# Optimization experiments

Measured on AMD Instinct MI355X. Metric: run time of the kernel, lower is better.

## Reference

```python
import jax, jax.numpy as jnp
import numpy as np

NUM_HEADS = 16

def setup_inputs() -> dict:
    key = jax.random.key(0)
    ks = jax.random.split(key, 9)
    B, S, H = 2, 2048, 1024
    sc = 0.02
    return {
        "x":  jax.random.normal(ks[0], (B, S, H), jnp.float32),
        "Wq": jax.random.normal(ks[1], (H, H), jnp.float32) * sc,
        "bq": jnp.zeros((H,), jnp.float32),
        "Wk": jax.random.normal(ks[2], (H, H), jnp.float32) * sc,
        "bk": jnp.zeros((H,), jnp.float32),
        "Wv": jax.random.normal(ks[3], (H, H), jnp.float32) * sc,
        "bv": jnp.zeros((H,), jnp.float32),
        "Wo": jax.random.normal(ks[4], (H, H), jnp.float32) * sc,
        "bo": jnp.zeros((H,), jnp.float32),
    }

def _split_heads(t, nh):
    B, S, H = t.shape
    return t.reshape(B, S, nh, H // nh).transpose(0, 2, 1, 3)  # [B, nh, S, hd]

def reference(x, Wq, bq, Wk, bk, Wv, bv, Wo, bo):
    # mask_type == 'gaussian', dropout = 0 (eval), return_weights = False
    B, S, H = x.shape
    nh = NUM_HEADS
    q = _split_heads(x @ Wq + bq, nh)  # [B, nh, S, hd]
    k = _split_heads(x @ Wk + bk, nh)
    v = _split_heads(x @ Wv + bv, nh)
    dif = q - k  # elementwise, as in the original
    # exp(-dif @ dif^T / 2)
    score = jnp.exp(-0.5 * jnp.einsum('bhqd,bhkd->bhqk', dif, dif))
    # gaussian mask: 1 strictly above the diagonal, 0 on/below (faithful to source)
    mask = jnp.triu(jnp.ones((S, S), x.dtype), k=1)
    prob = score * mask  # [B, nh, S, S]
    ctx = jnp.einsum('bhqk,bhkd->bhqd', prob, v)  # [B, nh, S, hd]
    ctx = ctx.transpose(0, 2, 1, 3).reshape(B, S, H)
    return ctx @ Wo + bo
```

## Files before the change

### kernel.cpp

```cpp
#include <hip/hip_runtime.h>
#include <math.h>

constexpr int SEQ  = 2048;
constexpr int HID  = 1024;
constexpr int MTOT = 4096;
constexpr int BH   = 32;

typedef _Float16 f16;
typedef _Float16 f16x8 __attribute__((ext_vector_type(8)));
typedef float    f32x4 __attribute__((ext_vector_type(4)));

__global__ __launch_bounds__(256) void cvt_x(const float* __restrict__ in,
                                             f16* __restrict__ out) {
    const int i = (blockIdx.x * 256 + threadIdx.x) * 4;
    float4 v = *(const float4*)(in + i);
    f16 o[4] = {(f16)v.x, (f16)v.y, (f16)v.z, (f16)v.w};
    *(ushort4*)(out + i) = *(ushort4*)o;
}

template<int SUB>
__global__ __launch_bounds__(256) void cvt_wT(const float* __restrict__ W,
                                              const float* __restrict__ W2,
                                              f16* __restrict__ WT) {
    __shared__ f16 T[64][72];
    const int k0 = blockIdx.x * 64, n0 = blockIdx.y * 64;
    const int t = threadIdx.x;
    const int r  = t >> 4;
    const int c4 = (t & 15) * 4;
#pragma unroll
    for (int rr = 0; rr < 64; rr += 16) {
        float4 w = *(const float4*)(W + (size_t)(k0 + rr + r) * HID + n0 + c4);
        if (SUB) {
            float4 w2 = *(const float4*)(W2 + (size_t)(k0 + rr + r) * HID + n0 + c4);
            w.x -= w2.x; w.y -= w2.y; w.z -= w2.z; w.w -= w2.w;
        }
        T[c4 + 0][rr + r] = (f16)w.x;
        T[c4 + 1][rr + r] = (f16)w.y;
        T[c4 + 2][rr + r] = (f16)w.z;
        T[c4 + 3][rr + r] = (f16)w.w;
    }
    __syncthreads();
#pragma unroll
    for (int pp = 0; pp < 2; pp++) {
        const int nr = pp * 32 + (t >> 3);
        const int kc = (t & 7) * 8;
        *(uint4*)(WT + (size_t)(n0 + nr) * HID + k0 + kc) = *(uint4*)(&T[nr][kc]);
    }
}

__global__ __launch_bounds__(256) void proj_gemm(const f16* __restrict__ A,
                                                 const f16* __restrict__ WqkT,
                                                 const f16* __restrict__ WvT,
                                                 const float* __restrict__ bq,
                                                 const float* __restrict__ bk,
                                                 const float* __restrict__ bv,
                                                 f16* __restrict__ dif,
                                                 f16* __restrict__ vT) {
    __shared__ f16 As[128 * 72];
    __shared__ f16 Bs[128 * 72];
    const int t = threadIdx.x;
    const int m0  = blockIdx.x * 128;
    const int n0g = blockIdx.y * 128;
    const bool isv = (n0g >= HID);
    const f16* BT = isv ? WvT : WqkT;
    const int n0 = n0g & (HID - 1);
    const int w = t >> 6, l = t & 63, quad = l >> 4, ln = l & 15;
    const int wm = (w >> 1) * 64, wn = (w & 1) * 64;
    const int srow = t >> 1, shalf = (t & 1) * 32;

    const f16* pa = A  + (size_t)(m0 + srow) * HID + shalf;
    const f16* pb = BT + (size_t)(n0 + srow) * HID + shalf;

    uint4 ar0 = *(const uint4*)(pa),      ar1 = *(const uint4*)(pa + 8);
    uint4 ar2 = *(const uint4*)(pa + 16), ar3 = *(const uint4*)(pa + 24);
    uint4 br0 = *(const uint4*)(pb),      br1 = *(const uint4*)(pb + 8);
    uint4 br2 = *(const uint4*)(pb + 16), br3 = *(const uint4*)(pb + 24);

    f32x4 acc[4][4] = {};

    for (int k0 = 0; k0 < HID; k0 += 64) {
        __syncthreads();
        f16* da = As + srow * 72 + shalf;
        f16* db = Bs + srow * 72 + shalf;
        *(uint4*)(da)      = ar0; *(uint4*)(da + 8)  = ar1;
        *(uint4*)(da + 16) = ar2; *(uint4*)(da + 24) = ar3;
        *(uint4*)(db)      = br0; *(uint4*)(db + 8)  = br1;
        *(uint4*)(db + 16) = br2; *(uint4*)(db + 24) = br3;
        __syncthreads();
        if (k0 + 64 < HID) {
            const f16* qa = pa + k0 + 64;
            const f16* qb = pb + k0 + 64;
            ar0 = *(const uint4*)(qa);      ar1 = *(const uint4*)(qa + 8);
            ar2 = *(const uint4*)(qa + 16); ar3 = *(const uint4*)(qa + 24);
            br0 = *(const uint4*)(qb);      br1 = *(const uint4*)(qb + 8);
            br2 = *(const uint4*)(qb + 16); br3 = *(const uint4*)(qb + 24);
        }
#pragma unroll
        for (int kh = 0; kh < 2; kh++) {
            f16x8 af[4], bf[4];
#pragma unroll
            for (int mt = 0; mt < 4; mt++)
                af[mt] = *(const f16x8*)(As + (wm + mt * 16 + ln) * 72 + kh * 32 + quad * 8);
#pragma unroll
            for (int nt = 0; nt < 4; nt++)
                bf[nt] = *(const f16x8*)(Bs + (wn + nt * 16 + ln) * 72 + kh * 32 + quad * 8);
#pragma unroll
            for (int mt = 0; mt < 4; mt++)
#pragma unroll
                for (int nt = 0; nt < 4; nt++)
                    acc[mt][nt] = __builtin_amdgcn_mfma_f32_16x16x32_f16(
                        af[mt], bf[nt], acc[mt][nt], 0, 0, 0);
        }
    }

#pragma unroll
    for (int mt = 0; mt < 4; mt++) {
#pragma unroll
        for (int nt = 0; nt < 4; nt++) {
            const int nl = n0 + wn + nt * 16 + ln;
            const int m_base = m0 + wm + mt * 16 + quad * 4;
            const int h = nl >> 6, e = nl & 63;
            if (!isv) {
                const float bb = bq[nl] - bk[nl];
#pragma unroll
                for (int r = 0; r < 4; r++) {
                    const int m = m_base + r;
                    const int b = m >> 11, s = m & 2047;
                    dif[((size_t)(b * 16 + h) * SEQ + s) * 64 + e] =
                        (f16)(acc[mt][nt][r] + bb);
                }
            } else {
                const float bb = bv[nl];
                const int b = m_base >> 11, s0 = m_base & 2047;
                f16 o[4];
#pragma unroll
                for (int r = 0; r < 4; r++) o[r] = (f16)(acc[mt][nt][r] + bb);
                *(ushort4*)(&vT[((size_t)(b * 16 + h) * 64 + e) * SEQ + s0]) =
                    *(ushort4*)o;
            }
        }
    }
}

__global__ __launch_bounds__(256) void out_gemm(const f16* __restrict__ C0,
                                                const f16* __restrict__ C1,
                                                const f16* __restrict__ WoT,
                                                const float* __restrict__ bo,
                                                float* __restrict__ out) {
    __shared__ f16 As[128 * 72];
    __shared__ f16 Bs[64 * 72];
    const int t = threadIdx.x;
    const int m0 = blockIdx.x * 128, n0 = blockIdx.y * 64;
    const int w = t >> 6, l = t & 63, quad = l >> 4, ln = l & 15;
    const int wm = (w >> 1) * 64, wn = (w & 1) * 32;
    const int arow = t >> 1, ahalf = (t & 1) * 32;
    const int brow = t >> 2, boff = (t & 3) * 16;

    const f16* pa0 = C0  + (size_t)(m0 + arow) * HID + ahalf;
    const f16* pa1 = C1  + (size_t)(m0 + arow) * HID + ahalf;
    const f16* pb  = WoT + (size_t)(n0 + brow) * HID + boff;

    f16x8 a0 = *(const f16x8*)(pa0)      + *(const f16x8*)(pa1);
    f16x8 a1 = *(const f16x8*)(pa0 + 8)  + *(const f16x8*)(pa1 + 8);
    f16x8 a2 = *(const f16x8*)(pa0 + 16) + *(const f16x8*)(pa1 + 16);
    f16x8 a3 = *(const f16x8*)(pa0 + 24) + *(const f16x8*)(pa1 + 24);
    uint4 b0 = *(const uint4*)(pb), b1 = *(const uint4*)(pb + 8);

    f32x4 acc[4][2] = {};

    for (int k0 = 0; k0 < HID; k0 += 64) {
        __syncthreads();
        f16* da = As + arow * 72 + ahalf;
        *(f16x8*)(da)      = a0; *(f16x8*)(da + 8)  = a1;
        *(f16x8*)(da + 16) = a2; *(f16x8*)(da + 24) = a3;
        f16* db = Bs + brow * 72 + boff;
        *(uint4*)(db) = b0; *(uint4*)(db + 8) = b1;
        __syncthreads();
        if (k0 + 64 < HID) {
            const int kn = k0 + 64;
            a0 = *(const f16x8*)(pa0 + kn)      + *(const f16x8*)(pa1 + kn);
            a1 = *(const f16x8*)(pa0 + kn + 8)  + *(const f16x8*)(pa1 + kn + 8);
            a2 = *(const f16x8*)(pa0 + kn + 16) + *(const f16x8*)(pa1 + kn + 16);
            a3 = *(const f16x8*)(pa0 + kn + 24) + *(const f16x8*)(pa1 + kn + 24);
            b0 = *(const uint4*)(pb + kn); b1 = *(const uint4*)(pb + kn + 8);
        }
#pragma unroll
        for (int kh = 0; kh < 2; kh++) {
            f16x8 af[4], bf[2];
#pragma unroll
            for (int mt = 0; mt < 4; mt++)
                af[mt] = *(const f16x8*)(As + (wm + mt * 16 + ln) * 72 + kh * 32 + quad * 8);
#pragma unroll
            for (int nt = 0; nt < 2; nt++)
                bf[nt] = *(const f16x8*)(Bs + (wn + nt * 16 + ln) * 72 + kh * 32 + quad * 8);
#pragma unroll
            for (int mt = 0; mt < 4; mt++)
#pragma unroll
                for (int nt = 0; nt < 2; nt++)
                    acc[mt][nt] = __builtin_amdgcn_mfma_f32_16x16x32_f16(
                        af[mt], bf[nt], acc[mt][nt], 0, 0, 0);
        }
    }

#pragma unroll
    for (int mt = 0; mt < 4; mt++)
#pragma unroll
        for (int nt = 0; nt < 2; nt++) {
            const int n = n0 + wn + nt * 16 + ln;
            const float bb = bo[n];
            const int m_base = m0 + wm + mt * 16 + quad * 4;
#pragma unroll
            for (int r = 0; r < 4; r++)
                out[(size_t)(m_base + r) * HID + n] =
                    acc[mt][nt][r] * 65536.0f + bb;
        }
}

__global__ __launch_bounds__(256) void attn_f16(const f16* __restrict__ dif,
                                                const f16* __restrict__ vT,
                                                f16* __restrict__ ctx0,
                                                f16* __restrict__ ctx1) {
    __shared__ f16 Qs[64 * 72];
    __shared__ f16 Ks[64 * 72];
    __shared__ f16 Vs[64 * 72];
    __shared__ f16 Ps[64 * 72];

    const int pq = blockIdx.x, bh = blockIdx.y, ks = blockIdx.z;
    f16* Cout = ks ? ctx1 : ctx0;
    const f16* D  = dif + (size_t)bh * SEQ * 64;
    const f16* VT = vT  + (size_t)bh * 64 * SEQ;
    const int b = bh >> 4, h = bh & 15;
    const int t = threadIdx.x, w = t >> 6, l = t & 63, quad = l >> 4, ln = l & 15;
    const int ve = t >> 2, vc = (t & 3) * 16;

    for (int half = 0; half < 2; half++) {
        const int qt = half ? (31 - pq) : pq;
        const int i0 = qt * 64;
        __syncthreads();

#pragma unroll
        for (int rr = 0; rr < 2; rr++) {
            const int o = rr * 2048 + t * 8;
            uint4 v = *(const uint4*)(D + i0 * 64 + o);
            *(uint4*)(Qs + (o >> 6) * 72 + (o & 63)) = v;
        }

        f32x4 acc[4] = {};
        const int kt0 = qt + ks;

        uint4 kr0, kr1, vr0, vr1;
        if (kt0 < 32) {
            const int j0 = kt0 * 64;
            kr0 = *(const uint4*)(D + j0 * 64 + t * 8);
            kr1 = *(const uint4*)(D + j0 * 64 + 2048 + t * 8);
            vr0 = *(const uint4*)(VT + (size_t)ve * SEQ + j0 + vc);
            vr1 = *(const uint4*)(VT + (size_t)ve * SEQ + j0 + vc + 8);
        }

        for (int kt = kt0; kt < 32; kt += 2) {
            __syncthreads();

            {
                const int o0 = t * 8, o1 = 2048 + t * 8;
                *(uint4*)(Ks + (o0 >> 6) * 72 + (o0 & 63)) = kr0;
                *(uint4*)(Ks + (o1 >> 6) * 72 + (o1 & 63)) = kr1;
                *(uint4*)(Vs + ve * 72 + vc)     = vr0;
                *(uint4*)(Vs + ve * 72 + vc + 8) = vr1;
            }
            __syncthreads();

            if (kt + 2 < 32) {
                const int j2 = (kt + 2) * 64;
                kr0 = *(const uint4*)(D + j2 * 64 + t * 8);
                kr1 = *(const uint4*)(D + j2 * 64 + 2048 + t * 8);
                vr0 = *(const uint4*)(VT + (size_t)ve * SEQ + j2 + vc);
                vr1 = *(const uint4*)(VT + (size_t)ve * SEQ + j2 + vc + 8);
            }

            f32x4 s[4] = {};
#pragma unroll
            for (int kh = 0; kh < 2; kh++) {
                f16x8 a = *(const f16x8*)(Qs + (w * 16 + ln) * 72 + kh * 32 + quad * 8);
#pragma unroll
                for (int nt = 0; nt < 4; nt++) {
                    f16x8 bfr = *(const f16x8*)(Ks + (nt * 16 + ln) * 72 + kh * 32 + quad * 8);
                    s[nt] = __builtin_amdgcn_mfma_f32_16x16x32_f16(a, bfr, s[nt], 0, 0, 0);
                }
            }

            const bool full = (kt > qt);
#pragma unroll
            for (int nt = 0; nt < 4; nt++)
#pragma unroll
                for (int r = 0; r < 4; r++) {
                    const int iloc = w * 16 + quad * 4 + r;
                    const int jloc = nt * 16 + ln;
                    float p = (full || (jloc > iloc))
                                  ? fminf(__expf(-0.5f * s[nt][r]) * 0x1p-16f, 60000.0f)
                                  : 0.0f;
                    Ps[iloc * 72 + jloc] = (f16)p;
                }

#pragma unroll
            for (int kh = 0; kh < 2; kh++) {
                f16x8 a = *(const f16x8*)(Ps + (w * 16 + ln) * 72 + kh * 32 + quad * 8);
#pragma unroll
                for (int nt = 0; nt < 4; nt++) {
                    f16x8 bfr = *(const f16x8*)(Vs + (nt * 16 + ln) * 72 + kh * 32 + quad * 8);
                    acc[nt] = __builtin_amdgcn_mfma_f32_16x16x32_f16(a, bfr, acc[nt], 0, 0, 0);
                }
            }
        }

#pragma unroll
        for (int nt = 0; nt < 4; nt++)
#pragma unroll
            for (int r = 0; r < 4; r++) {
                const int iloc = w * 16 + quad * 4 + r;
                Cout[(size_t)(b * SEQ + i0 + iloc) * HID + h * 64 + nt * 16 + ln] =
                    (f16)acc[nt][r];
            }
    }
}

extern "C" void kernel_launch(void* const* d_in, const int* in_sizes, int n_in,
                              void* d_out, int out_size, void* d_ws, size_t ws_size,
                              hipStream_t stream) {
    const float* x  = (const float*)d_in[0];
    const float* Wq = (const float*)d_in[1];
    const float* bq = (const float*)d_in[2];
    const float* Wk = (const float*)d_in[3];
    const float* bk = (const float*)d_in[4];
    const float* Wv = (const float*)d_in[5];
    const float* bv = (const float*)d_in[6];
    const float* Wo = (const float*)d_in[7];
    const float* bo = (const float*)d_in[8];
    float* out = (float*)d_out;

    char* ws = (char*)d_ws;
    f16* xh   = (f16*)(ws);
    f16* WqkT = (f16*)(ws + (8 << 20));
    f16* WvT  = (f16*)(ws + (10 << 20));
    f16* WoT  = (f16*)(ws + (12 << 20));
    f16* dif  = (f16*)(ws + (14 << 20));
    f16* vT   = (f16*)(ws + (22 << 20));
    f16* ctx0 = (f16*)(ws + (30 << 20));
    f16* ctx1 = (f16*)(ws + (38 << 20));

    cvt_x<<<MTOT * HID / 1024, 256, 0, stream>>>(x, xh);
    dim3 wtg(16, 16);
    cvt_wT<1><<<wtg, 256, 0, stream>>>(Wq, Wk, WqkT);
    cvt_wT<0><<<wtg, 256, 0, stream>>>(Wv, nullptr, WvT);
    cvt_wT<0><<<wtg, 256, 0, stream>>>(Wo, nullptr, WoT);

    proj_gemm<<<dim3(MTOT / 128, 16), 256, 0, stream>>>(xh, WqkT, WvT,
                                                        bq, bk, bv, dif, vT);
    attn_f16<<<dim3(16, BH, 2), 256, 0, stream>>>(dif, vT, ctx0, ctx1);
    out_gemm<<<dim3(MTOT / 128, 16), 256, 0, stream>>>(ctx0, ctx1, WoT, bo, out);
}
```

Before: 191.4 us.

## Use 128-row query tiles with three-way key split in attention

```diff
diff --git a/kernel.cpp b/kernel.cpp
--- a/kernel.cpp
+++ b/kernel.cpp
@@ -18,11 +18,19 @@
     *(ushort4*)(out + i) = *(ushort4*)o;
 }
 
-template<int SUB>
-__global__ __launch_bounds__(256) void cvt_wT(const float* __restrict__ W,
-                                              const float* __restrict__ W2,
-                                              f16* __restrict__ WT) {
+__global__ __launch_bounds__(256) void cvt_w_all(const float* __restrict__ Wq,
+                                                 const float* __restrict__ Wk,
+                                                 const float* __restrict__ Wv,
+                                                 const float* __restrict__ Wo,
+                                                 f16* __restrict__ WqkT,
+                                                 f16* __restrict__ WvT,
+                                                 f16* __restrict__ WoT) {
     __shared__ f16 T[64][72];
+    const int z = blockIdx.z;
+    const float* W  = (z == 0) ? Wq : (z == 1) ? Wv : Wo;
+    const float* W2 = Wk;
+    f16* WT = (z == 0) ? WqkT : (z == 1) ? WvT : WoT;
+
     const int k0 = blockIdx.x * 64, n0 = blockIdx.y * 64;
     const int t = threadIdx.x;
     const int r  = t >> 4;
@@ -30,7 +38,7 @@
 #pragma unroll
     for (int rr = 0; rr < 64; rr += 16) {
         float4 w = *(const float4*)(W + (size_t)(k0 + rr + r) * HID + n0 + c4);
-        if (SUB) {
+        if (z == 0) {
             float4 w2 = *(const float4*)(W2 + (size_t)(k0 + rr + r) * HID + n0 + c4);
             w.x -= w2.x; w.y -= w2.y; w.z -= w2.z; w.w -= w2.w;
         }
@@ -144,6 +152,7 @@
 
 __global__ __launch_bounds__(256) void out_gemm(const f16* __restrict__ C0,
                                                 const f16* __restrict__ C1,
+                                                const f16* __restrict__ C2,
                                                 const f16* __restrict__ WoT,
                                                 const float* __restrict__ bo,
                                                 float* __restrict__ out) {
@@ -158,12 +167,13 @@
 
     const f16* pa0 = C0  + (size_t)(m0 + arow) * HID + ahalf;
     const f16* pa1 = C1  + (size_t)(m0 + arow) * HID + ahalf;
+    const f16* pa2 = C2  + (size_t)(m0 + arow) * HID + ahalf;
     const f16* pb  = WoT + (size_t)(n0 + brow) * HID + boff;
 
-    f16x8 a0 = *(const f16x8*)(pa0)      + *(const f16x8*)(pa1);
-    f16x8 a1 = *(const f16x8*)(pa0 + 8)  + *(const f16x8*)(pa1 + 8);
-    f16x8 a2 = *(const f16x8*)(pa0 + 16) + *(const f16x8*)(pa1 + 16);
-    f16x8 a3 = *(const f16x8*)(pa0 + 24) + *(const f16x8*)(pa1 + 24);
+    f16x8 a0 = *(const f16x8*)(pa0)      + *(const f16x8*)(pa1)      + *(const f16x8*)(pa2);
+    f16x8 a1 = *(const f16x8*)(pa0 + 8)  + *(const f16x8*)(pa1 + 8)  + *(const f16x8*)(pa2 + 8);
+    f16x8 a2 = *(const f16x8*)(pa0 + 16) + *(const f16x8*)(pa1 + 16) + *(const f16x8*)(pa2 + 16);
+    f16x8 a3 = *(const f16x8*)(pa0 + 24) + *(const f16x8*)(pa1 + 24) + *(const f16x8*)(pa2 + 24);
     uint4 b0 = *(const uint4*)(pb), b1 = *(const uint4*)(pb + 8);
 
     f32x4 acc[4][2] = {};
@@ -178,10 +188,10 @@
         __syncthreads();
         if (k0 + 64 < HID) {
             const int kn = k0 + 64;
-            a0 = *(const f16x8*)(pa0 + kn)      + *(const f16x8*)(pa1 + kn);
-            a1 = *(const f16x8*)(pa0 + kn + 8)  + *(const f16x8*)(pa1 + kn + 8);
-            a2 = *(const f16x8*)(pa0 + kn + 16) + *(const f16x8*)(pa1 + kn + 16);
-            a3 = *(const f16x8*)(pa0 + kn + 24) + *(const f16x8*)(pa1 + kn + 24);
+            a0 = *(const f16x8*)(pa0 + kn)      + *(const f16x8*)(pa1 + kn)      + *(const f16x8*)(pa2 + kn);
+            a1 = *(const f16x8*)(pa0 + kn + 8)  + *(const f16x8*)(pa1 + kn + 8)  + *(const f16x8*)(pa2 + kn + 8);
+            a2 = *(const f16x8*)(pa0 + kn + 16) + *(const f16x8*)(pa1 + kn + 16) + *(const f16x8*)(pa2 + kn + 16);
+            a3 = *(const f16x8*)(pa0 + kn + 24) + *(const f16x8*)(pa1 + kn + 24) + *(const f16x8*)(pa2 + kn + 24);
             b0 = *(const uint4*)(pb + kn); b1 = *(const uint4*)(pb + kn + 8);
         }
 #pragma unroll
@@ -219,14 +229,16 @@
 __global__ __launch_bounds__(256) void attn_f16(const f16* __restrict__ dif,
                                                 const f16* __restrict__ vT,
                                                 f16* __restrict__ ctx0,
-                                                f16* __restrict__ ctx1) {
-    __shared__ f16 Qs[64 * 72];
-    __shared__ f16 Ks[64 * 72];
-    __shared__ f16 Vs[64 * 72];
-    __shared__ f16 Ps[64 * 72];
+                                                f16* __restrict__ ctx1,
+                                                f16* __restrict__ ctx2) {
+    constexpr int LP = 72;
+    __shared__ f16 KV[2 * 64 * LP];
+    __shared__ f16 Ps[128 * LP];
+    f16* Ks = KV;
+    f16* Vs = KV + 64 * LP;
 
     const int pq = blockIdx.x, bh = blockIdx.y, ks = blockIdx.z;
-    f16* Cout = ks ? ctx1 : ctx0;
+    f16* Cout = (ks == 0) ? ctx0 : (ks == 1) ? ctx1 : ctx2;
     const f16* D  = dif + (size_t)bh * SEQ * 64;
     const f16* VT = vT  + (size_t)bh * 64 * SEQ;
     const int b = bh >> 4, h = bh & 15;
@@ -234,92 +246,121 @@
     const int ve = t >> 2, vc = (t & 3) * 16;
 
     for (int half = 0; half < 2; half++) {
-        const int qt = half ? (31 - pq) : pq;
-        const int i0 = qt * 64;
-        __syncthreads();
-
-#pragma unroll
-        for (int rr = 0; rr < 2; rr++) {
-            const int o = rr * 2048 + t * 8;
-            uint4 v = *(const uint4*)(D + i0 * 64 + o);
-            *(uint4*)(Qs + (o >> 6) * 72 + (o & 63)) = v;
-        }
-
-        f32x4 acc[4] = {};
-        const int kt0 = qt + ks;
+        const int qt = half ? (15 - pq) : pq;
+        const int i0 = qt * 128;
+        __syncthreads();
+
+#pragma unroll
+        for (int c = 0; c < 4; c++) {
+            const int o = c * 2048 + t * 8;
+            *(uint4*)(&KV[o]) = *(const uint4*)(D + (size_t)i0 * 64 + o);
+        }
+        __syncthreads();
+        f16x8 aq[2][2];
+#pragma unroll
+        for (int st = 0; st < 2; st++)
+#pragma unroll
+            for (int kh = 0; kh < 2; kh++)
+                aq[st][kh] = *(const f16x8*)(&KV[(w * 32 + st * 16 + ln) * 64
+                                                + kh * 32 + quad * 8]);
+        __syncthreads();
+
+        f32x4 acc[2][4] = {};
+        const int kt0 = qt * 2 + ks;
 
         uint4 kr0, kr1, vr0, vr1;
         if (kt0 < 32) {
             const int j0 = kt0 * 64;
-            kr0 = *(const uint4*)(D + j0 * 64 + t * 8);
-            kr1 = *(const uint4*)(D + j0 * 64 + 2048 + t * 8);
+            kr0 = *(const uint4*)(D + (size_t)j0 * 64 + t * 8);
+            kr1 = *(const uint4*)(D + (size_t)j0 * 64 + 2048 + t * 8);
             vr0 = *(const uint4*)(VT + (size_t)ve * SEQ + j0 + vc);
             vr1 = *(const uint4*)(VT + (size_t)ve * SEQ + j0 + vc + 8);
         }
 
-        for (int kt = kt0; kt < 32; kt += 2) {
+        for (int kt = kt0; kt < 32; kt += 3) {
+            const int j0 = kt * 64;
             __syncthreads();
 
             {
                 const int o0 = t * 8, o1 = 2048 + t * 8;
-                *(uint4*)(Ks + (o0 >> 6) * 72 + (o0 & 63)) = kr0;
-                *(uint4*)(Ks + (o1 >> 6) * 72 + (o1 & 63)) = kr1;
-                *(uint4*)(Vs + ve * 72 + vc)     = vr0;
-                *(uint4*)(Vs + ve * 72 + vc + 8) = vr1;
+                *(uint4*)(&Ks[(o0 >> 6) * LP + (o0 & 63)]) = kr0;
+                *(uint4*)(&Ks[(o1 >> 6) * LP + (o1 & 63)]) = kr1;
+                *(uint4*)(&Vs[ve * LP + vc])     = vr0;
+                *(uint4*)(&Vs[ve * LP + vc + 8]) = vr1;
             }
             __syncthreads();
 
-            if (kt + 2 < 32) {
-                const int j2 = (kt + 2) * 64;
-                kr0 = *(const uint4*)(D + j2 * 64 + t * 8);
-                kr1 = *(const uint4*)(D + j2 * 64 + 2048 + t * 8);
+            if (kt + 3 < 32) {
+                const int j2 = (kt + 3) * 64;
+                kr0 = *(const uint4*)(D + (size_t)j2 * 64 + t * 8);
+                kr1 = *(const uint4*)(D + (size_t)j2 * 64 + 2048 + t * 8);
                 vr0 = *(const uint4*)(VT + (size_t)ve * SEQ + j2 + vc);
                 vr1 = *(const uint4*)(VT + (size_t)ve * SEQ + j2 + vc + 8);
             }
 
-            f32x4 s[4] = {};
+            const int gi0 = i0 + w * 32;
+            const bool live0 = (j0 + 63) > gi0;
+            const bool live1 = (j0 + 63) > (gi0 + 16);
+
+            f32x4 s[2][4] = {};
+#pragma unroll
+            for (int kh = 0; kh < 2; kh++)
+#pragma unroll
+                for (int nt = 0; nt < 4; nt++) {
+                    f16x8 bk = *(const f16x8*)(&Ks[(nt * 16 + ln) * LP + kh * 32 + quad * 8]);
+                    if (live0) s[0][nt] = __builtin_amdgcn_mfma_f32_16x16x32_f16(
+                                              aq[0][kh], bk, s[0][nt], 0, 0, 0);
+                    if (live1) s[1][nt] = __builtin_amdgcn_mfma_f32_16x16x32_f16(
+                                              aq[1][kh], bk, s[1][nt], 0, 0, 0);
+                }
+
+#pragma unroll
+            for (int st = 0; st < 2; st++) {
+                const bool live = st ? live1 : live0;
+                if (!live) continue;
+                const int gs = gi0 + st * 16;
+                const bool nomask = j0 > gs + 15;
+#pragma unroll
+                for (int nt = 0; nt < 4; nt++)
+#pragma unroll
+                    for (int r = 0; r < 4; r++) {
+                        float p = __expf(fmaf(s[st][nt][r], -0.5f, -11.090354888959125f));
+                        p = fminf(p, 60000.0f);
+                        if (!nomask) {
+                            const int gi = gs + quad * 4 + r;
+                            const int gj = j0 + nt * 16 + ln;
+                            p = (gj > gi) ? p : 0.0f;
+                        }
+                        Ps[(w * 32 + st * 16 + quad * 4 + r) * LP + nt * 16 + ln] = (f16)p;
+                    }
+            }
+
 #pragma unroll
             for (int kh = 0; kh < 2; kh++) {
-                f16x8 a = *(const f16x8*)(Qs + (w * 16 + ln) * 72 + kh * 32 + quad * 8);
+                f16x8 ap0, ap1;
+                if (live0) ap0 = *(const f16x8*)(&Ps[(w * 32 + ln) * LP + kh * 32 + quad * 8]);
+                if (live1) ap1 = *(const f16x8*)(&Ps[(w * 32 + 16 + ln) * LP + kh * 32 + quad * 8]);
 #pragma unroll
                 for (int nt = 0; nt < 4; nt++) {
-                    f16x8 bfr = *(const f16x8*)(Ks + (nt * 16 + ln) * 72 + kh * 32 + quad * 8);
-                    s[nt] = __builtin_amdgcn_mfma_f32_16x16x32_f16(a, bfr, s[nt], 0, 0, 0);
+                    f16x8 bv = *(const f16x8*)(&Vs[(nt * 16 + ln) * LP + kh * 32 + quad * 8]);
+                    if (live0) acc[0][nt] = __builtin_amdgcn_mfma_f32_16x16x32_f16(
+                                                ap0, bv, acc[0][nt], 0, 0, 0);
+                    if (live1) acc[1][nt] = __builtin_amdgcn_mfma_f32_16x16x32_f16(
+                                                ap1, bv, acc[1][nt], 0, 0, 0);
                 }
             }
-
-            const bool full = (kt > qt);
+        }
+
+#pragma unroll
+        for (int st = 0; st < 2; st++)
 #pragma unroll
             for (int nt = 0; nt < 4; nt++)
 #pragma unroll
                 for (int r = 0; r < 4; r++) {
-                    const int iloc = w * 16 + quad * 4 + r;
-                    const int jloc = nt * 16 + ln;
-                    float p = (full || (jloc > iloc))
-                                  ? fminf(__expf(-0.5f * s[nt][r]) * 0x1p-16f, 60000.0f)
-                                  : 0.0f;
-                    Ps[iloc * 72 + jloc] = (f16)p;
+                    const int iloc = w * 32 + st * 16 + quad * 4 + r;
+                    Cout[(size_t)(b * SEQ + i0 + iloc) * HID + h * 64 + nt * 16 + ln] =
+                        (f16)acc[st][nt][r];
                 }
-
-#pragma unroll
-            for (int kh = 0; kh < 2; kh++) {
-                f16x8 a = *(const f16x8*)(Ps + (w * 16 + ln) * 72 + kh * 32 + quad * 8);
-#pragma unroll
-                for (int nt = 0; nt < 4; nt++) {
-                    f16x8 bfr = *(const f16x8*)(Vs + (nt * 16 + ln) * 72 + kh * 32 + quad * 8);
-                    acc[nt] = __builtin_amdgcn_mfma_f32_16x16x32_f16(a, bfr, acc[nt], 0, 0, 0);
-                }
-            }
-        }
-
-#pragma unroll
-        for (int nt = 0; nt < 4; nt++)
-#pragma unroll
-            for (int r = 0; r < 4; r++) {
-                const int iloc = w * 16 + quad * 4 + r;
-                Cout[(size_t)(b * SEQ + i0 + iloc) * HID + h * 64 + nt * 16 + ln] =
-                    (f16)acc[nt][r];
-            }
     }
 }
 
@@ -346,15 +387,13 @@
     f16* vT   = (f16*)(ws + (22 << 20));
     f16* ctx0 = (f16*)(ws + (30 << 20));
     f16* ctx1 = (f16*)(ws + (38 << 20));
+    f16* ctx2 = xh;
 
     cvt_x<<<MTOT * HID / 1024, 256, 0, stream>>>(x, xh);
-    dim3 wtg(16, 16);
-    cvt_wT<1><<<wtg, 256, 0, stream>>>(Wq, Wk, WqkT);
-    cvt_wT<0><<<wtg, 256, 0, stream>>>(Wv, nullptr, WvT);
-    cvt_wT<0><<<wtg, 256, 0, stream>>>(Wo, nullptr, WoT);
+    cvt_w_all<<<dim3(16, 16, 3), 256, 0, stream>>>(Wq, Wk, Wv, Wo, WqkT, WvT, WoT);
 
     proj_gemm<<<dim3(MTOT / 128, 16), 256, 0, stream>>>(xh, WqkT, WvT,
                                                         bq, bk, bv, dif, vT);
-    attn_f16<<<dim3(16, BH, 2), 256, 0, stream>>>(dif, vT, ctx0, ctx1);
-    out_gemm<<<dim3(MTOT / 128, 16), 256, 0, stream>>>(ctx0, ctx1, WoT, bo, out);
-}
+    attn_f16<<<dim3(8, BH, 3), 256, 0, stream>>>(dif, vT, ctx0, ctx1, ctx2);
+    out_gemm<<<dim3(MTOT / 128, 16), 256, 0, stream>>>(ctx0, ctx1, ctx2, WoT, bo, out);
+}
```

After: 205.5 us. +7.3%, slower.

## Merge conversion kernels into one launch and double-buffer LDS in GEMMs

Applied to the files above, without the earlier changes.

```diff
diff --git a/kernel.cpp b/kernel.cpp
--- a/kernel.cpp
+++ b/kernel.cpp
@@ -10,28 +10,43 @@
 typedef _Float16 f16x8 __attribute__((ext_vector_type(8)));
 typedef float    f32x4 __attribute__((ext_vector_type(4)));
 
-__global__ __launch_bounds__(256) void cvt_x(const float* __restrict__ in,
-                                             f16* __restrict__ out) {
-    const int i = (blockIdx.x * 256 + threadIdx.x) * 4;
-    float4 v = *(const float4*)(in + i);
-    f16 o[4] = {(f16)v.x, (f16)v.y, (f16)v.z, (f16)v.w};
-    *(ushort4*)(out + i) = *(ushort4*)o;
-}
-
-template<int SUB>
-__global__ __launch_bounds__(256) void cvt_wT(const float* __restrict__ W,
-                                              const float* __restrict__ W2,
-                                              f16* __restrict__ WT) {
+__global__ __launch_bounds__(256) void prep(const float* __restrict__ x,
+                                            const float* __restrict__ Wq,
+                                            const float* __restrict__ Wk,
+                                            const float* __restrict__ Wv,
+                                            const float* __restrict__ Wo,
+                                            f16* __restrict__ xh,
+                                            f16* __restrict__ WqkT,
+                                            f16* __restrict__ WvT,
+                                            f16* __restrict__ WoT) {
     __shared__ f16 T[64][72];
+    const int z = blockIdx.z;
+    const int t = threadIdx.x;
+
+    if (z == 3) {
+        const int chunk = blockIdx.y * 16 + blockIdx.x;
+        const float* src = x + (size_t)chunk * 16384;
+        f16* dst = xh + (size_t)chunk * 16384;
+#pragma unroll
+        for (int it = 0; it < 16; it++) {
+            const int i = it * 1024 + t * 4;
+            float4 v = *(const float4*)(src + i);
+            f16 o[4] = {(f16)v.x, (f16)v.y, (f16)v.z, (f16)v.w};
+            *(ushort4*)(dst + i) = *(ushort4*)o;
+        }
+        return;
+    }
+
+    const float* W  = (z == 0) ? Wq : (z == 1) ? Wv : Wo;
+    f16* WT = (z == 0) ? WqkT : (z == 1) ? WvT : WoT;
     const int k0 = blockIdx.x * 64, n0 = blockIdx.y * 64;
-    const int t = threadIdx.x;
     const int r  = t >> 4;
     const int c4 = (t & 15) * 4;
 #pragma unroll
     for (int rr = 0; rr < 64; rr += 16) {
         float4 w = *(const float4*)(W + (size_t)(k0 + rr + r) * HID + n0 + c4);
-        if (SUB) {
-            float4 w2 = *(const float4*)(W2 + (size_t)(k0 + rr + r) * HID + n0 + c4);
+        if (z == 0) {
+            float4 w2 = *(const float4*)(Wk + (size_t)(k0 + rr + r) * HID + n0 + c4);
             w.x -= w2.x; w.y -= w2.y; w.z -= w2.z; w.w -= w2.w;
         }
         T[c4 + 0][rr + r] = (f16)w.x;
@@ -56,8 +71,8 @@
                                                  const float* __restrict__ bv,
                                                  f16* __restrict__ dif,
                                                  f16* __restrict__ vT) {
-    __shared__ f16 As[128 * 72];
-    __shared__ f16 Bs[128 * 72];
+    __shared__ f16 As[2][128 * 72];
+    __shared__ f16 Bs[2][128 * 72];
     const int t = threadIdx.x;
     const int m0  = blockIdx.x * 128;
     const int n0g = blockIdx.y * 128;
@@ -77,11 +92,11 @@
     uint4 br2 = *(const uint4*)(pb + 16), br3 = *(const uint4*)(pb + 24);
 
     f32x4 acc[4][4] = {};
+    int buf = 0;
 
     for (int k0 = 0; k0 < HID; k0 += 64) {
-        __syncthreads();
-        f16* da = As + srow * 72 + shalf;
-        f16* db = Bs + srow * 72 + shalf;
+        f16* da = As[buf] + srow * 72 + shalf;
+        f16* db = Bs[buf] + srow * 72 + shalf;
         *(uint4*)(da)      = ar0; *(uint4*)(da + 8)  = ar1;
         *(uint4*)(da + 16) = ar2; *(uint4*)(da + 24) = ar3;
         *(uint4*)(db)      = br0; *(uint4*)(db + 8)  = br1;
@@ -100,10 +115,10 @@
             f16x8 af[4], bf[4];
 #pragma unroll
             for (int mt = 0; mt < 4; mt++)
-                af[mt] = *(const f16x8*)(As + (wm + mt * 16 + ln) * 72 + kh * 32 + quad * 8);
+                af[mt] = *(const f16x8*)(As[buf] + (wm + mt * 16 + ln) * 72 + kh * 32 + quad * 8);
 #pragma unroll
             for (int nt = 0; nt < 4; nt++)
-                bf[nt] = *(const f16x8*)(Bs + (wn + nt * 16 + ln) * 72 + kh * 32 + quad * 8);
+                bf[nt] = *(const f16x8*)(Bs[buf] + (wn + nt * 16 + ln) * 72 + kh * 32 + quad * 8);
 #pragma unroll
             for (int mt = 0; mt < 4; mt++)
 #pragma unroll
@@ -111,6 +126,7 @@
                     acc[mt][nt] = __builtin_amdgcn_mfma_f32_16x16x32_f16(
                         af[mt], bf[nt], acc[mt][nt], 0, 0, 0);
         }
+        buf ^= 1;
     }
 
 #pragma unroll
@@ -147,8 +163,8 @@
                                                 const f16* __restrict__ WoT,
                                                 const float* __restrict__ bo,
                                                 float* __restrict__ out) {
-    __shared__ f16 As[128 * 72];
-    __shared__ f16 Bs[64 * 72];
+    __shared__ f16 As[2][128 * 72];
+    __shared__ f16 Bs[2][64 * 72];
     const int t = threadIdx.x;
     const int m0 = blockIdx.x * 128, n0 = blockIdx.y * 64;
     const int w = t >> 6, l = t & 63, quad = l >> 4, ln = l & 15;
@@ -167,13 +183,13 @@
     uint4 b0 = *(const uint4*)(pb), b1 = *(const uint4*)(pb + 8);
 
     f32x4 acc[4][2] = {};
+    int buf = 0;
 
     for (int k0 = 0; k0 < HID; k0 += 64) {
-        __syncthreads();
-        f16* da = As + arow * 72 + ahalf;
+        f16* da = As[buf] + arow * 72 + ahalf;
         *(f16x8*)(da)      = a0; *(f16x8*)(da + 8)  = a1;
         *(f16x8*)(da + 16) = a2; *(f16x8*)(da + 24) = a3;
-        f16* db = Bs + brow * 72 + boff;
+        f16* db = Bs[buf] + brow * 72 + boff;
         *(uint4*)(db) = b0; *(uint4*)(db + 8) = b1;
         __syncthreads();
         if (k0 + 64 < HID) {
@@ -189,10 +205,10 @@
             f16x8 af[4], bf[2];
 #pragma unroll
             for (int mt = 0; mt < 4; mt++)
-                af[mt] = *(const f16x8*)(As + (wm + mt * 16 + ln) * 72 + kh * 32 + quad * 8);
+                af[mt] = *(const f16x8*)(As[buf] + (wm + mt * 16 + ln) * 72 + kh * 32 + quad * 8);
 #pragma unroll
             for (int nt = 0; nt < 2; nt++)
-                bf[nt] = *(const f16x8*)(Bs + (wn + nt * 16 + ln) * 72 + kh * 32 + quad * 8);
+                bf[nt] = *(const f16x8*)(Bs[buf] + (wn + nt * 16 + ln) * 72 + kh * 32 + quad * 8);
 #pragma unroll
             for (int mt = 0; mt < 4; mt++)
 #pragma unroll
@@ -200,6 +216,7 @@
                     acc[mt][nt] = __builtin_amdgcn_mfma_f32_16x16x32_f16(
                         af[mt], bf[nt], acc[mt][nt], 0, 0, 0);
         }
+        buf ^= 1;
     }
 
 #pragma unroll
@@ -347,12 +364,8 @@
     f16* ctx0 = (f16*)(ws + (30 << 20));
     f16* ctx1 = (f16*)(ws + (38 << 20));
 
-    cvt_x<<<MTOT * HID / 1024, 256, 0, stream>>>(x, xh);
-    dim3 wtg(16, 16);
-    cvt_wT<1><<<wtg, 256, 0, stream>>>(Wq, Wk, WqkT);
-    cvt_wT<0><<<wtg, 256, 0, stream>>>(Wv, nullptr, WvT);
-    cvt_wT<0><<<wtg, 256, 0, stream>>>(Wo, nullptr, WoT);
-
+    prep<<<dim3(16, 16, 4), 256, 0, stream>>>(x, Wq, Wk, Wv, Wo,
+                                              xh, WqkT, WvT, WoT);
     proj_gemm<<<dim3(MTOT / 128, 16), 256, 0, stream>>>(xh, WqkT, WvT,
                                                         bq, bk, bv, dif, vT);
     attn_f16<<<dim3(16, BH, 2), 256, 0, stream>>>(dif, vT, ctx0, ctx1);
```

New measurement: 188.0 us. Within noise of the previous version (-1.8%).
